# Optimization experiments

Measured on AMD Instinct MI355X. Metric: run time of the kernel, lower is better.

Reference implementation:

```python
import jax, jax.numpy as jnp
import numpy as np

H = 16  # n_heads

def setup_inputs() -> dict:
    key = jax.random.key(0)
    k1, k2, k3, k4 = jax.random.split(key, 4)
    B, S, D = 2, 2048, 1024
    query = jax.random.normal(k1, (B, S, D), dtype=jnp.float32)
    pos_emb = jax.random.normal(k2, (S, D), dtype=jnp.float32)
    w_qkv = jax.random.normal(k3, (D, 3 * D), dtype=jnp.float32) * (D ** -0.5)
    w_out = jax.random.normal(k4, (D, D), dtype=jnp.float32) * (D ** -0.5)
    return {"query": query, "pos_emb": pos_emb, "w_qkv": w_qkv, "w_out": w_out}

def reference(query, pos_emb, w_qkv, w_out):
    B, S, D = query.shape
    d_k = D // H
    # ape=True: pos_fn applied to input before QKV projection (additive APE)
    x = query + pos_emb[None, :, :]
    # fused QKV projection; torch view(B,S,H,3*d_k) + chunk(3,-1) == reshape(B,S,H,3,d_k)
    qkv = jnp.einsum('bsd,de->bse', x, w_qkv).reshape(B, S, H, 3, d_k)
    qkv = jnp.transpose(qkv, (0, 2, 1, 3, 4))  # [B,H,S,3,d_k]
    q, k, v = qkv[..., 0, :], qkv[..., 1, :], qkv[..., 2, :]
    scale = d_k ** -0.5
    scores = jnp.einsum('bhqd,bhkd->bhqk', q, k) * scale  # [B,H,S,S]
    attn = jax.nn.softmax(scores, axis=-1)  # dropout is identity in eval
    o = jnp.einsum('bhqk,bhkd->bhqd', attn, v)
    o = jnp.transpose(o, (0, 2, 1, 3)).reshape(B, S, D)
    return jnp.einsum('bsd,de->bse', o, w_out)
```

## Files before the change

kernel.cpp:

```cpp
#include <hip/hip_runtime.h>

#define SS 2048
#define DD 1024
#define N3 3072

typedef unsigned short u16;
typedef unsigned int u32;
typedef __attribute__((ext_vector_type(8))) short bf16x8;
typedef __attribute__((ext_vector_type(4))) short bf16x4;
typedef __attribute__((ext_vector_type(4))) float f32x4;

__device__ __forceinline__ u16 f2bf(float f) {
    u32 u = __float_as_uint(f);
    u32 r = u + 0x7fffu + ((u >> 16) & 1u);
    return (u16)(r >> 16);
}

__device__ __forceinline__ float fast_exp2(float x) {
    return __builtin_amdgcn_exp2f(x);
}

__device__ __forceinline__ void async_cp16(u16* lds, const u16* g) {
    __builtin_amdgcn_global_load_lds((const __attribute__((address_space(1))) u32*)g,
                                     (__attribute__((address_space(3))) u32*)lds, 16, 0, 0);
}

__device__ __forceinline__ f32x4 mfma16(bf16x4 a, bf16x4 b, f32x4 c) {
    return __builtin_amdgcn_mfma_f32_16x16x16bf16_1k(a, b, c, 0, 0, 0);
}

__global__ __launch_bounds__(256)
void prep_all(const float* __restrict__ q, const float* __restrict__ pos,
              const float* __restrict__ wqkv, const float* __restrict__ wout,
              u16* __restrict__ x, u16* __restrict__ wqkvT, u16* __restrict__ woutT)
{
    __shared__ float t[32][33];
    const int bx = blockIdx.x;

    if (bx < 4096) {
        const size_t i = ((size_t)bx * 256 + threadIdx.x) * 4;
        float4 a = *(const float4*)(q + i);
        float4 p = *(const float4*)(pos + (i & (size_t)(SS * DD - 1)));
        uint2 r;
        r.x = (u32)f2bf(a.x + p.x) | ((u32)f2bf(a.y + p.y) << 16);
        r.y = (u32)f2bf(a.z + p.z) | ((u32)f2bf(a.w + p.w) << 16);
        *(uint2*)(x + i) = r;
        return;
    }

    const int isq = bx < 7168;
    const int tt  = isq ? (bx - 4096) : (bx - 7168);
    const int nx  = isq ? 96 : 32;
    const int N   = isq ? N3 : DD;
    const float* W = isq ? wqkv : wout;
    u16* WT = isq ? wqkvT : woutT;

    const int x0 = (tt % nx) * 32, y0 = (tt / nx) * 32;
    const int tx = threadIdx.x & 31, ty = threadIdx.x >> 5;
#pragma unroll
    for (int i = 0; i < 4; ++i)
        t[ty + i * 8][tx] = W[(size_t)(y0 + ty + i * 8) * N + x0 + tx];
    __syncthreads();
#pragma unroll
    for (int i = 0; i < 4; ++i) {
        const int n = x0 + ty + i * 8;
        float v = t[tx][ty + i * 8];
        if (isq && (n % 192) < 64) v *= 0.18033688f;
        WT[(size_t)n * DD + y0 + tx] = f2bf(v);
    }
}

__global__ __launch_bounds__(256)
void transpose_v(const u16* __restrict__ qkv, u16* __restrict__ vt)
{
    __shared__ u16 t[64][72];
    const int bx = blockIdx.x;
    const int bh = bx >> 5, st = bx & 31;
    const int b = bh >> 4, h = bh & 15;
    const int r = threadIdx.x >> 2, c16 = (threadIdx.x & 3) * 16;

    const u16* src = qkv + (size_t)(b * SS + st * 64 + r) * N3 + h * 192 + 128 + c16;
    *(uint4*)&t[r][c16]     = *(const uint4*)src;
    *(uint4*)&t[r][c16 + 8] = *(const uint4*)(src + 8);
    __syncthreads();

    union { uint4 q[2]; u16 hh[16]; } u;
#pragma unroll
    for (int j = 0; j < 16; ++j) u.hh[j] = t[c16 + j][r];
    uint4* dst = (uint4*)(vt + ((size_t)bh * 64 + r) * SS + st * 64 + c16);
    dst[0] = u.q[0]; dst[1] = u.q[1];
}

__global__ __launch_bounds__(512, 2)
void gemm256(const u16* __restrict__ A, const u16* __restrict__ BT,
             u16* __restrict__ C, int M, int N, int K)
{
    extern __shared__ __align__(16) u16 smem[];

    const int tid = threadIdx.x;
    const int lane = tid & 63;
    const int wv = tid >> 6;
    const int quad = lane >> 4, l16 = lane & 15;
    const int wm = wv >> 2, wn = wv & 3;
    const int m0 = blockIdx.y * 256, n0 = blockIdx.x * 256;
    const int sw = l16 & 7;

    const int srow = tid >> 3, pc = tid & 7, lc = pc ^ (srow & 7);
    const u16* agp = A  + (size_t)(m0 + srow) * K + lc * 8;
    const u16* bgp = BT + (size_t)(n0 + srow) * K + lc * 8;
    u16* const asw = smem +         srow * 64 + pc * 8;
    u16* const bsw = smem + 32768 + srow * 64 + pc * 8;

    auto stage = [&](int buf, int k0) {
#pragma unroll
        for (int s = 0; s < 4; ++s)
            async_cp16(asw + buf * 16384 + s * 4096, agp + (size_t)(s * 64) * K + k0);
#pragma unroll
        for (int s = 0; s < 4; ++s)
            async_cp16(bsw + buf * 16384 + s * 4096, bgp + (size_t)(s * 64) * K + k0);
    };

    f32x4 acc[8][4];
#pragma unroll
    for (int i = 0; i < 8; ++i)
#pragma unroll
        for (int j = 0; j < 4; ++j) acc[i][j] = {0.f, 0.f, 0.f, 0.f};

    stage(0, 0);

    const int NT = K / 64;
    for (int t = 0; t < NT; ++t) {
        const int p = t & 1;
        asm volatile("s_waitcnt vmcnt(0) lgkmcnt(0)\n\ts_barrier" ::: "memory");
        if (t + 1 < NT) stage(p ^ 1, (t + 1) * 64);

        const u16* Ab = smem +         p * 16384;
        const u16* Bb = smem + 32768 + p * 16384;

#pragma unroll
        for (int ks = 0; ks < 2; ++ks) {
            bf16x8 bfr[4];
#pragma unroll
            for (int nt = 0; nt < 4; ++nt)
                bfr[nt] = *(const bf16x8*)&Bb[(wn * 64 + nt * 16 + l16) * 64 + (((ks * 4 + quad) ^ sw) << 3)];
#pragma unroll
            for (int mt = 0; mt < 8; ++mt) {
                bf16x8 af = *(const bf16x8*)&Ab[(wm * 128 + mt * 16 + l16) * 64 + (((ks * 4 + quad) ^ sw) << 3)];
#pragma unroll
                for (int nt = 0; nt < 4; ++nt)
                    acc[mt][nt] = __builtin_amdgcn_mfma_f32_16x16x32_bf16(af, bfr[nt], acc[mt][nt], 0, 0, 0);
            }
        }
    }

#pragma unroll
    for (int mt = 0; mt < 8; ++mt)
#pragma unroll
        for (int r = 0; r < 4; ++r) {
            const size_t row = m0 + wm * 128 + mt * 16 + quad * 4 + r;
            u16* cp = C + row * N + n0 + wn * 64 + l16;
#pragma unroll
            for (int nt = 0; nt < 4; ++nt) cp[nt * 16] = f2bf(acc[mt][nt][r]);
        }
}

template <int OUT_BF16, int NT>
__global__ __launch_bounds__(256)
void gemm_mfma(const u16* __restrict__ A, const u16* __restrict__ BT,
               void* __restrict__ Cv, int M, int N, int K)
{
    constexpr int FR = NT / 32;
    __shared__ u16 As[128 * 64];
    __shared__ u16 Bs[NT * 64];

    const int tid = threadIdx.x;
    const int lane = tid & 63, wv = tid >> 6;
    const int quad = lane >> 4, l16 = lane & 15;
    const int m0 = blockIdx.y * 128, n0 = blockIdx.x * NT;

    const int arow = wv * 32 + (lane >> 3);
    const int pc   = lane & 7;
    const int lcA  = pc ^ (arow & 7);
    const u16* agp = A + (size_t)(m0 + arow) * K + lcA * 8;
    u16* alp = As + arow * 64 + pc * 8;

    const int brow = (NT == 128) ? (wv * 32 + (lane >> 3)) : (wv * 8 + (lane >> 3));
    const int lcB  = pc ^ (brow & 7);
    const u16* bgp = BT + (size_t)(n0 + brow) * K + lcB * 8;
    u16* blp = Bs + brow * 64 + pc * 8;

    const int moff = (wv >> 1) * 64, noff = (wv & 1) * (NT / 2);

    f32x4 acc[4][FR];
#pragma unroll
    for (int i = 0; i < 4; ++i)
#pragma unroll
        for (int j = 0; j < FR; ++j) acc[i][j] = {0.f, 0.f, 0.f, 0.f};

    const int swf = l16 & 7;

    for (int k0 = 0; k0 < K; k0 += 64) {
#pragma unroll
        for (int s = 0; s < 4; ++s)
            async_cp16(alp + s * 8 * 64, agp + (size_t)(s * 8) * K + k0);
        if constexpr (NT == 128) {
#pragma unroll
            for (int s = 0; s < 4; ++s)
                async_cp16(blp + s * 8 * 64, bgp + (size_t)(s * 8) * K + k0);
        } else {
#pragma unroll
            for (int s = 0; s < 2; ++s)
                async_cp16(blp + s * 32 * 64, bgp + (size_t)(s * 32) * K + k0);
        }
        __syncthreads();

#pragma unroll
        for (int ks = 0; ks < 2; ++ks) {
            bf16x8 af[4], bfr[FR];
#pragma unroll
            for (int t = 0; t < 4; ++t)
                af[t] = *(const bf16x8*)&As[(moff + t * 16 + l16) * 64 + (((ks * 4 + quad) ^ swf) << 3)];
#pragma unroll
            for (int t = 0; t < FR; ++t)
                bfr[t] = *(const bf16x8*)&Bs[(noff + t * 16 + l16) * 64 + (((ks * 4 + quad) ^ swf) << 3)];
#pragma unroll
            for (int mt = 0; mt < 4; ++mt)
#pragma unroll
                for (int nt = 0; nt < FR; ++nt)
                    acc[mt][nt] = __builtin_amdgcn_mfma_f32_16x16x32_bf16(af[mt], bfr[nt], acc[mt][nt], 0, 0, 0);
        }
        __syncthreads();
    }

#pragma unroll
    for (int mt = 0; mt < 4; ++mt)
#pragma unroll
        for (int r = 0; r < 4; ++r) {
            const size_t row = m0 + moff + mt * 16 + quad * 4 + r;
            if (OUT_BF16) {
                u16* cp = (u16*)Cv + row * N + n0 + noff + l16;
#pragma unroll
                for (int nt = 0; nt < FR; ++nt) cp[nt * 16] = f2bf(acc[mt][nt][r]);
            } else {
                float* cp = (float*)Cv + row * N + n0 + noff + l16;
#pragma unroll
                for (int nt = 0; nt < FR; ++nt) cp[nt * 16] = acc[mt][nt][r];
            }
        }
}

__global__ __launch_bounds__(512, 4)
void attn_mfma(const u16* __restrict__ qkv, const u16* __restrict__ vt, u16* __restrict__ o)
{
    __shared__ __align__(16) u16 smem[32768];

    const int tid = threadIdx.x;
    const int lane = tid & 63, wv = tid >> 6;
    const int grp = wv >> 2, w4 = wv & 3;
    const int quad = lane >> 4, l16 = lane & 15;
    const int bx = blockIdx.x;
    const int bh = bx & 31, qt = bx >> 5;
    const int h = bh & 15, b = bh >> 4;

    const size_t hb = (size_t)b * SS * N3 + h * 192;
    const int q0 = qt * 128 + w4 * 32;
    const int sw = l16 & 7;

    bf16x8 qf[2][2];
#pragma unroll
    for (int mt = 0; mt < 2; ++mt)
#pragma unroll
        for (int ks = 0; ks < 2; ++ks)
            qf[mt][ks] = *(const bf16x8*)(qkv + hb + (size_t)(q0 + mt * 16 + l16) * N3 + ks * 32 + quad * 8);

    f32x4 po[2][4];
#pragma unroll
    for (int mt = 0; mt < 2; ++mt)
#pragma unroll
        for (int nt = 0; nt < 4; ++nt) po[mt][nt] = {0.f, 0.f, 0.f, 0.f};
    float lrun[2] = {0.f, 0.f};

    const int lrow = lane >> 3, pc8 = lane & 7, lc = pc8 ^ lrow;
    const int srow = w4 * 16;
    const int kt0 = grp * 16;

    const u16* kgp = qkv + hb + 64 + (size_t)(kt0 * 64 + srow + lrow) * N3 + lc * 8;
    const u16* vgp = vt + ((size_t)bh * 64 + srow + lrow) * SS + kt0 * 64 + lc * 8;

    u16* const ksA = smem + (grp * 2) * 4096 + (srow + lrow) * 64 + pc8 * 8;
    u16* const ksB = ksA + 4096;
    u16* const vsA = smem + 16384 + (grp * 2) * 4096 + (srow + lrow) * 64 + pc8 * 8;
    u16* const vsB = vsA + 4096;

    async_cp16(ksA,       kgp);
    async_cp16(ksA + 512, kgp + (size_t)8 * N3);
    async_cp16(vsA,       vgp);
    async_cp16(vsA + 512, vgp + (size_t)8 * SS);

    for (int it = 0; it < 16; ++it) {
        const int p = it & 1;
        asm volatile("s_waitcnt vmcnt(0) lgkmcnt(0)\n\ts_barrier" ::: "memory");
        if (it < 15) {
            const size_t ko = (size_t)(it + 1) * 64;
            u16* kb = p ? ksA : ksB;
            u16* vb = p ? vsA : vsB;
            async_cp16(kb,       kgp + ko * N3);
            async_cp16(kb + 512, kgp + ko * N3 + (size_t)8 * N3);
            async_cp16(vb,       vgp + ko);
            async_cp16(vb + 512, vgp + ko + (size_t)8 * SS);
        }
        const u16* kbuf = smem + (grp * 2 + p) * 4096;
        const u16* vbuf = smem + 16384 + (grp * 2 + p) * 4096;

        f32x4 sf[2][4];
#pragma unroll
        for (int mt = 0; mt < 2; ++mt)
#pragma unroll
            for (int kn = 0; kn < 4; ++kn) sf[mt][kn] = {0.f, 0.f, 0.f, 0.f};
        __builtin_amdgcn_s_setprio(1);
#pragma unroll
        for (int ks = 0; ks < 2; ++ks)
#pragma unroll
            for (int kn = 0; kn < 4; ++kn) {
                bf16x8 kf = *(const bf16x8*)&kbuf[(kn * 16 + l16) * 64 + (((ks * 4 + quad) ^ sw) << 3)];
#pragma unroll
                for (int mt = 0; mt < 2; ++mt)
                    sf[mt][kn] = __builtin_amdgcn_mfma_f32_16x16x32_bf16(kf, qf[mt][ks], sf[mt][kn], 0, 0, 0);
            }
        __builtin_amdgcn_s_setprio(0);

        u32 SW[2][4][2];
#pragma unroll
        for (int mt = 0; mt < 2; ++mt) {
            float ls = 0.f;
#pragma unroll
            for (int kn = 0; kn < 4; ++kn) {
                const float p0 = fast_exp2(sf[mt][kn][0]);
                const float p1 = fast_exp2(sf[mt][kn][1]);
                const float p2 = fast_exp2(sf[mt][kn][2]);
                const float p3 = fast_exp2(sf[mt][kn][3]);
                ls += (p0 + p1) + (p2 + p3);
                SW[mt][kn][0] = __builtin_amdgcn_perm(__float_as_uint(p1), __float_as_uint(p0), 0x07060302u);
                SW[mt][kn][1] = __builtin_amdgcn_perm(__float_as_uint(p3), __float_as_uint(p2), 0x07060302u);
            }
            lrun[mt] += ls;
        }

        __builtin_amdgcn_s_setprio(1);
#pragma unroll
        for (int kn = 0; kn < 4; ++kn) {
            bf16x4 vf[4];
#pragma unroll
            for (int nt = 0; nt < 4; ++nt)
                vf[nt] = *(const bf16x4*)&vbuf[(nt * 16 + l16) * 64 + (((2 * kn + (quad >> 1)) ^ sw) << 3) + ((quad & 1) << 2)];
#pragma unroll
            for (int mt = 0; mt < 2; ++mt) {
                union { bf16x4 v; u32 w[2]; } pu;
                pu.w[0] = SW[mt][kn][0];
                pu.w[1] = SW[mt][kn][1];
#pragma unroll
                for (int nt = 0; nt < 4; ++nt)
                    po[mt][nt] = mfma16(vf[nt], pu.v, po[mt][nt]);
            }
        }
        __builtin_amdgcn_s_setprio(0);
    }

    __syncthreads();

#pragma unroll
    for (int mt = 0; mt < 2; ++mt) {
        lrun[mt] += __shfl_xor(lrun[mt], 16, 64);
        lrun[mt] += __shfl_xor(lrun[mt], 32, 64);
    }

    float* xch = (float*)smem;
    if (grp == 1) {
        float* d = xch + (w4 * 64 + lane) * 36;
#pragma unroll
        for (int mt = 0; mt < 2; ++mt)
#pragma unroll
            for (int nt = 0; nt < 4; ++nt)
                *(f32x4*)(d + mt * 16 + nt * 4) = po[mt][nt];
        d[32] = lrun[0]; d[33] = lrun[1];
    }
    __syncthreads();
    if (grp == 0) {
        const float* s = xch + (w4 * 64 + lane) * 36;
#pragma unroll
        for (int mt = 0; mt < 2; ++mt)
#pragma unroll
            for (int nt = 0; nt < 4; ++nt)
                po[mt][nt] = po[mt][nt] + *(const f32x4*)(s + mt * 16 + nt * 4);
        lrun[0] += s[32]; lrun[1] += s[33];

#pragma unroll
        for (int mt = 0; mt < 2; ++mt) {
            const float linv = 1.f / lrun[mt];
            const size_t row = (size_t)b * SS + q0 + mt * 16 + l16;
#pragma unroll
            for (int nt = 0; nt < 4; ++nt) {
                const u32 h0 = (u32)f2bf(po[mt][nt][0] * linv) | ((u32)f2bf(po[mt][nt][1] * linv) << 16);
                const u32 h1 = (u32)f2bf(po[mt][nt][2] * linv) | ((u32)f2bf(po[mt][nt][3] * linv) << 16);
                uint2 wp; wp.x = h0; wp.y = h1;
                *(uint2*)(o + row * DD + h * 64 + nt * 16 + quad * 4) = wp;
            }
        }
    }
}

extern "C" void kernel_launch(void* const* d_in, const int* in_sizes, int n_in,
                              void* d_out, int out_size, void* d_ws, size_t ws_size,
                              hipStream_t stream)
{
    const float* query  = (const float*)d_in[0];
    const float* posemb = (const float*)d_in[1];
    const float* w_qkv  = (const float*)d_in[2];
    const float* w_out  = (const float*)d_in[3];
    float* out = (float*)d_out;

    u16* xb    = (u16*)d_ws;
    u16* wqkvT = xb    + (size_t)4096 * 1024;
    u16* woutT = wqkvT + (size_t)3072 * 1024;
    u16* qkv   = woutT + (size_t)1024 * 1024;
    u16* ob    = qkv   + (size_t)4096 * 3072;
    u16* vtb   = ob    + (size_t)4096 * 1024;

    static bool lds_init = false;
    if (!lds_init) {
        hipFuncSetAttribute((const void*)gemm256,
                            hipFuncAttributeMaxDynamicSharedMemorySize, 131072);
        lds_init = true;
    }

    prep_all<<<8192, 256, 0, stream>>>(query, posemb, w_qkv, w_out, xb, wqkvT, woutT);

    gemm256<<<dim3(N3 / 256, 4096 / 256), 512, 131072, stream>>>(xb, wqkvT, qkv, 4096, N3, DD);

    transpose_v<<<1024, 256, 0, stream>>>(qkv, vtb);

    attn_mfma<<<dim3(512, 1, 1), 512, 0, stream>>>(qkv, vtb, ob);

    gemm_mfma<0, 64><<<dim3(DD / 64, 4096 / 128), 256, 0, stream>>>(ob, woutT, (void*)out, 4096, DD, DD);
}
```

Measured before the change: 185.2 us.

## Fuse V transpose into QKV GEMM epilogue, regroup weight columns, swizzle blocks

Result: no change. 184.7 us (-0.3%).

```diff
diff --git a/kernel.cpp b/kernel.cpp
--- a/kernel.cpp
+++ b/kernel.cpp
@@ -64,45 +64,36 @@
 #pragma unroll
     for (int i = 0; i < 4; ++i) {
         const int n = x0 + ty + i * 8;
+        int dst = n;
+        if (isq) {
+            const int hh = n / 192, r = n % 192;
+            dst = (r < 64) ? hh * 64 + r
+                : (r < 128) ? 1024 + hh * 64 + (r - 64)
+                            : 2048 + hh * 64 + (r - 128);
+        }
         float v = t[tx][ty + i * 8];
-        if (isq && (n % 192) < 64) v *= 0.18033688f;
-        WT[(size_t)n * DD + y0 + tx] = f2bf(v);
-    }
-}
-
-__global__ __launch_bounds__(256)
-void transpose_v(const u16* __restrict__ qkv, u16* __restrict__ vt)
-{
-    __shared__ u16 t[64][72];
-    const int bx = blockIdx.x;
-    const int bh = bx >> 5, st = bx & 31;
-    const int b = bh >> 4, h = bh & 15;
-    const int r = threadIdx.x >> 2, c16 = (threadIdx.x & 3) * 16;
-
-    const u16* src = qkv + (size_t)(b * SS + st * 64 + r) * N3 + h * 192 + 128 + c16;
-    *(uint4*)&t[r][c16]     = *(const uint4*)src;
-    *(uint4*)&t[r][c16 + 8] = *(const uint4*)(src + 8);
-    __syncthreads();
-
-    union { uint4 q[2]; u16 hh[16]; } u;
-#pragma unroll
-    for (int j = 0; j < 16; ++j) u.hh[j] = t[c16 + j][r];
-    uint4* dst = (uint4*)(vt + ((size_t)bh * 64 + r) * SS + st * 64 + c16);
-    dst[0] = u.q[0]; dst[1] = u.q[1];
+        if (isq && dst < 1024) v *= 0.18033688f;
+        WT[(size_t)dst * DD + y0 + tx] = f2bf(v);
+    }
 }
 
 __global__ __launch_bounds__(512, 2)
 void gemm256(const u16* __restrict__ A, const u16* __restrict__ BT,
-             u16* __restrict__ C, int M, int N, int K)
+             u16* __restrict__ C, u16* __restrict__ vt, int M, int N, int K, int nbx)
 {
     extern __shared__ __align__(16) u16 smem[];
+
+    const int bid = blockIdx.x;
+    const int chunk = (int)gridDim.x >> 3;
+    const int swz = (bid & 7) * chunk + (bid >> 3);
+    const int bxs = swz % nbx, bys = swz / nbx;
 
     const int tid = threadIdx.x;
     const int lane = tid & 63;
     const int wv = tid >> 6;
     const int quad = lane >> 4, l16 = lane & 15;
     const int wm = wv >> 2, wn = wv & 3;
-    const int m0 = blockIdx.y * 256, n0 = blockIdx.x * 256;
+    const int m0 = bys * 256, n0 = bxs * 256;
     const int sw = l16 & 7;
 
     const int srow = tid >> 3, pc = tid & 7, lc = pc ^ (srow & 7);
@@ -153,30 +144,61 @@
         }
     }
 
-#pragma unroll
-    for (int mt = 0; mt < 8; ++mt)
-#pragma unroll
-        for (int r = 0; r < 4; ++r) {
-            const size_t row = m0 + wm * 128 + mt * 16 + quad * 4 + r;
-            u16* cp = C + row * N + n0 + wn * 64 + l16;
-#pragma unroll
-            for (int nt = 0; nt < 4; ++nt) cp[nt * 16] = f2bf(acc[mt][nt][r]);
-        }
+    if (vt && n0 >= 2048) {
+        __syncthreads();
+        u16* tb = smem;
+#pragma unroll
+        for (int mt = 0; mt < 8; ++mt)
+#pragma unroll
+            for (int nt = 0; nt < 4; ++nt) {
+                const int vl = wn * 64 + nt * 16 + l16;
+                const int ml = wm * 128 + mt * 16 + quad * 4;
+                uint2 w;
+                w.x = (u32)f2bf(acc[mt][nt][0]) | ((u32)f2bf(acc[mt][nt][1]) << 16);
+                w.y = (u32)f2bf(acc[mt][nt][2]) | ((u32)f2bf(acc[mt][nt][3]) << 16);
+                *(uint2*)(tb + (size_t)vl * 264 + ml) = w;
+            }
+        __syncthreads();
+        const int vl = tid >> 1, half = tid & 1;
+        const int b16 = (m0 >> 11) * 16;
+        const int hh = ((n0 - 2048) >> 6) + (vl >> 6);
+        const int dk = vl & 63;
+        u16* dst = vt + ((size_t)(b16 + hh) * 64 + dk) * SS + (m0 & 2047) + half * 128;
+        const u16* src = tb + (size_t)vl * 264 + half * 128;
+#pragma unroll
+        for (int j = 0; j < 16; ++j)
+            *(uint4*)(dst + j * 8) = *(const uint4*)(src + j * 8);
+    } else {
+#pragma unroll
+        for (int mt = 0; mt < 8; ++mt)
+#pragma unroll
+            for (int r = 0; r < 4; ++r) {
+                const size_t row = m0 + wm * 128 + mt * 16 + quad * 4 + r;
+                u16* cp = C + row * N + n0 + wn * 64 + l16;
+#pragma unroll
+                for (int nt = 0; nt < 4; ++nt) cp[nt * 16] = f2bf(acc[mt][nt][r]);
+            }
+    }
 }
 
 template <int OUT_BF16, int NT>
 __global__ __launch_bounds__(256)
 void gemm_mfma(const u16* __restrict__ A, const u16* __restrict__ BT,
-               void* __restrict__ Cv, int M, int N, int K)
+               void* __restrict__ Cv, int M, int N, int K, int nbx)
 {
     constexpr int FR = NT / 32;
     __shared__ u16 As[128 * 64];
     __shared__ u16 Bs[NT * 64];
 
+    const int bid = blockIdx.x;
+    const int chunk = (int)gridDim.x >> 3;
+    const int swz = (bid & 7) * chunk + (bid >> 3);
+    const int bxs = swz % nbx, bys = swz / nbx;
+
     const int tid = threadIdx.x;
     const int lane = tid & 63, wv = tid >> 6;
     const int quad = lane >> 4, l16 = lane & 15;
-    const int m0 = blockIdx.y * 128, n0 = blockIdx.x * NT;
+    const int m0 = bys * 128, n0 = bxs * NT;
 
     const int arow = wv * 32 + (lane >> 3);
     const int pc   = lane & 7;
@@ -262,7 +284,7 @@
     const int bh = bx & 31, qt = bx >> 5;
     const int h = bh & 15, b = bh >> 4;
 
-    const size_t hb = (size_t)b * SS * N3 + h * 192;
+    const size_t base = (size_t)b * SS * N3;
     const int q0 = qt * 128 + w4 * 32;
     const int sw = l16 & 7;
 
@@ -271,7 +293,7 @@
     for (int mt = 0; mt < 2; ++mt)
 #pragma unroll
         for (int ks = 0; ks < 2; ++ks)
-            qf[mt][ks] = *(const bf16x8*)(qkv + hb + (size_t)(q0 + mt * 16 + l16) * N3 + ks * 32 + quad * 8);
+            qf[mt][ks] = *(const bf16x8*)(qkv + base + h * 64 + (size_t)(q0 + mt * 16 + l16) * N3 + ks * 32 + quad * 8);
 
     f32x4 po[2][4];
 #pragma unroll
@@ -284,7 +306,7 @@
     const int srow = w4 * 16;
     const int kt0 = grp * 16;
 
-    const u16* kgp = qkv + hb + 64 + (size_t)(kt0 * 64 + srow + lrow) * N3 + lc * 8;
+    const u16* kgp = qkv + base + 1024 + h * 64 + (size_t)(kt0 * 64 + srow + lrow) * N3 + lc * 8;
     const u16* vgp = vt + ((size_t)bh * 64 + srow + lrow) * SS + kt0 * 64 + lc * 8;
 
     u16* const ksA = smem + (grp * 2) * 4096 + (srow + lrow) * 64 + pc8 * 8;
@@ -429,17 +451,15 @@
     static bool lds_init = false;
     if (!lds_init) {
         hipFuncSetAttribute((const void*)gemm256,
-                            hipFuncAttributeMaxDynamicSharedMemorySize, 131072);
+                            hipFuncAttributeMaxDynamicSharedMemorySize, 135168);
         lds_init = true;
     }
 
     prep_all<<<8192, 256, 0, stream>>>(query, posemb, w_qkv, w_out, xb, wqkvT, woutT);
 
-    gemm256<<<dim3(N3 / 256, 4096 / 256), 512, 131072, stream>>>(xb, wqkvT, qkv, 4096, N3, DD);
-
-    transpose_v<<<1024, 256, 0, stream>>>(qkv, vtb);
+    gemm256<<<192, 512, 135168, stream>>>(xb, wqkvT, qkv, vtb, 4096, N3, DD, N3 / 256);
 
     attn_mfma<<<dim3(512, 1, 1), 512, 0, stream>>>(qkv, vtb, ob);
 
-    gemm_mfma<0, 64><<<dim3(DD / 64, 4096 / 128), 256, 0, stream>>>(ob, woutT, (void*)out, 4096, DD, DD);
-}
+    gemm_mfma<0, 64><<<512, 256, 0, stream>>>(ob, woutT, (void*)out, 4096, DD, DD, DD / 64);
+}
```

## Retile QKV GEMM to 128x192 tiles, reorder QKV columns, swizzle block IDs

Applied to the files above, without the earlier changes.

Result: no change. 186.5 us (+0.7%).

```diff
diff --git a/kernel.cpp b/kernel.cpp
--- a/kernel.cpp
+++ b/kernel.cpp
@@ -64,9 +64,16 @@
 #pragma unroll
     for (int i = 0; i < 4; ++i) {
         const int n = x0 + ty + i * 8;
+        int dst = n;
+        if (isq) {
+            const int hh = n / 192, r = n % 192;
+            dst = (r < 64) ? hh * 64 + r
+                : (r < 128) ? 1024 + hh * 64 + (r - 64)
+                            : 2048 + hh * 64 + (r - 128);
+        }
         float v = t[tx][ty + i * 8];
-        if (isq && (n % 192) < 64) v *= 0.18033688f;
-        WT[(size_t)n * DD + y0 + tx] = f2bf(v);
+        if (isq && dst < 1024) v *= 0.18033688f;
+        WT[(size_t)dst * DD + y0 + tx] = f2bf(v);
     }
 }
 
@@ -79,7 +86,7 @@
     const int b = bh >> 4, h = bh & 15;
     const int r = threadIdx.x >> 2, c16 = (threadIdx.x & 3) * 16;
 
-    const u16* src = qkv + (size_t)(b * SS + st * 64 + r) * N3 + h * 192 + 128 + c16;
+    const u16* src = qkv + (size_t)(b * SS + st * 64 + r) * N3 + 2048 + h * 64 + c16;
     *(uint4*)&t[r][c16]     = *(const uint4*)src;
     *(uint4*)&t[r][c16 + 8] = *(const uint4*)(src + 8);
     __syncthreads();
@@ -92,39 +99,44 @@
 }
 
 __global__ __launch_bounds__(512, 2)
-void gemm256(const u16* __restrict__ A, const u16* __restrict__ BT,
-             u16* __restrict__ C, int M, int N, int K)
+void gemm192(const u16* __restrict__ A, const u16* __restrict__ BT,
+             u16* __restrict__ C, int M, int N, int K, int nbx)
 {
     extern __shared__ __align__(16) u16 smem[];
+
+    const int bid = blockIdx.x;
+    const int chunk = (int)gridDim.x >> 3;
+    const int swz = (bid & 7) * chunk + (bid >> 3);
+    const int bxs = swz % nbx, bys = swz / nbx;
 
     const int tid = threadIdx.x;
     const int lane = tid & 63;
     const int wv = tid >> 6;
     const int quad = lane >> 4, l16 = lane & 15;
     const int wm = wv >> 2, wn = wv & 3;
-    const int m0 = blockIdx.y * 256, n0 = blockIdx.x * 256;
+    const int m0 = bys * 128, n0 = bxs * 192;
     const int sw = l16 & 7;
 
     const int srow = tid >> 3, pc = tid & 7, lc = pc ^ (srow & 7);
     const u16* agp = A  + (size_t)(m0 + srow) * K + lc * 8;
     const u16* bgp = BT + (size_t)(n0 + srow) * K + lc * 8;
     u16* const asw = smem +         srow * 64 + pc * 8;
-    u16* const bsw = smem + 32768 + srow * 64 + pc * 8;
+    u16* const bsw = smem + 16384 + srow * 64 + pc * 8;
 
     auto stage = [&](int buf, int k0) {
 #pragma unroll
-        for (int s = 0; s < 4; ++s)
-            async_cp16(asw + buf * 16384 + s * 4096, agp + (size_t)(s * 64) * K + k0);
-#pragma unroll
-        for (int s = 0; s < 4; ++s)
-            async_cp16(bsw + buf * 16384 + s * 4096, bgp + (size_t)(s * 64) * K + k0);
+        for (int s = 0; s < 2; ++s)
+            async_cp16(asw + buf * 8192 + s * 4096, agp + (size_t)(s * 64) * K + k0);
+#pragma unroll
+        for (int s = 0; s < 3; ++s)
+            async_cp16(bsw + buf * 12288 + s * 4096, bgp + (size_t)(s * 64) * K + k0);
     };
 
-    f32x4 acc[8][4];
-#pragma unroll
-    for (int i = 0; i < 8; ++i)
-#pragma unroll
-        for (int j = 0; j < 4; ++j) acc[i][j] = {0.f, 0.f, 0.f, 0.f};
+    f32x4 acc[4][3];
+#pragma unroll
+    for (int i = 0; i < 4; ++i)
+#pragma unroll
+        for (int j = 0; j < 3; ++j) acc[i][j] = {0.f, 0.f, 0.f, 0.f};
 
     stage(0, 0);
 
@@ -134,49 +146,57 @@
         asm volatile("s_waitcnt vmcnt(0) lgkmcnt(0)\n\ts_barrier" ::: "memory");
         if (t + 1 < NT) stage(p ^ 1, (t + 1) * 64);
 
-        const u16* Ab = smem +         p * 16384;
-        const u16* Bb = smem + 32768 + p * 16384;
+        const u16* Ab = smem +         p * 8192;
+        const u16* Bb = smem + 16384 + p * 12288;
 
 #pragma unroll
         for (int ks = 0; ks < 2; ++ks) {
-            bf16x8 bfr[4];
-#pragma unroll
-            for (int nt = 0; nt < 4; ++nt)
-                bfr[nt] = *(const bf16x8*)&Bb[(wn * 64 + nt * 16 + l16) * 64 + (((ks * 4 + quad) ^ sw) << 3)];
-#pragma unroll
-            for (int mt = 0; mt < 8; ++mt) {
-                bf16x8 af = *(const bf16x8*)&Ab[(wm * 128 + mt * 16 + l16) * 64 + (((ks * 4 + quad) ^ sw) << 3)];
-#pragma unroll
-                for (int nt = 0; nt < 4; ++nt)
-                    acc[mt][nt] = __builtin_amdgcn_mfma_f32_16x16x32_bf16(af, bfr[nt], acc[mt][nt], 0, 0, 0);
-            }
-        }
-    }
-
-#pragma unroll
-    for (int mt = 0; mt < 8; ++mt)
+            bf16x8 bfr[3], af[4];
+#pragma unroll
+            for (int nt = 0; nt < 3; ++nt)
+                bfr[nt] = *(const bf16x8*)&Bb[(wn * 48 + nt * 16 + l16) * 64 + (((ks * 4 + quad) ^ sw) << 3)];
+#pragma unroll
+            for (int mt = 0; mt < 4; ++mt)
+                af[mt] = *(const bf16x8*)&Ab[(wm * 64 + mt * 16 + l16) * 64 + (((ks * 4 + quad) ^ sw) << 3)];
+            __builtin_amdgcn_s_setprio(1);
+#pragma unroll
+            for (int mt = 0; mt < 4; ++mt)
+#pragma unroll
+                for (int nt = 0; nt < 3; ++nt)
+                    acc[mt][nt] = __builtin_amdgcn_mfma_f32_16x16x32_bf16(af[mt], bfr[nt], acc[mt][nt], 0, 0, 0);
+            __builtin_amdgcn_s_setprio(0);
+        }
+    }
+
+#pragma unroll
+    for (int mt = 0; mt < 4; ++mt)
 #pragma unroll
         for (int r = 0; r < 4; ++r) {
-            const size_t row = m0 + wm * 128 + mt * 16 + quad * 4 + r;
-            u16* cp = C + row * N + n0 + wn * 64 + l16;
-#pragma unroll
-            for (int nt = 0; nt < 4; ++nt) cp[nt * 16] = f2bf(acc[mt][nt][r]);
+            const size_t row = m0 + wm * 64 + mt * 16 + quad * 4 + r;
+            u16* cp = C + row * N + n0 + wn * 48 + l16;
+#pragma unroll
+            for (int nt = 0; nt < 3; ++nt) cp[nt * 16] = f2bf(acc[mt][nt][r]);
         }
 }
 
 template <int OUT_BF16, int NT>
 __global__ __launch_bounds__(256)
 void gemm_mfma(const u16* __restrict__ A, const u16* __restrict__ BT,
-               void* __restrict__ Cv, int M, int N, int K)
+               void* __restrict__ Cv, int M, int N, int K, int nbx)
 {
     constexpr int FR = NT / 32;
     __shared__ u16 As[128 * 64];
     __shared__ u16 Bs[NT * 64];
 
+    const int bid = blockIdx.x;
+    const int chunk = (int)gridDim.x >> 3;
+    const int swz = (bid & 7) * chunk + (bid >> 3);
+    const int bxs = swz % nbx, bys = swz / nbx;
+
     const int tid = threadIdx.x;
     const int lane = tid & 63, wv = tid >> 6;
     const int quad = lane >> 4, l16 = lane & 15;
-    const int m0 = blockIdx.y * 128, n0 = blockIdx.x * NT;
+    const int m0 = bys * 128, n0 = bxs * NT;
 
     const int arow = wv * 32 + (lane >> 3);
     const int pc   = lane & 7;
@@ -262,7 +282,7 @@
     const int bh = bx & 31, qt = bx >> 5;
     const int h = bh & 15, b = bh >> 4;
 
-    const size_t hb = (size_t)b * SS * N3 + h * 192;
+    const size_t base = (size_t)b * SS * N3;
     const int q0 = qt * 128 + w4 * 32;
     const int sw = l16 & 7;
 
@@ -271,7 +291,7 @@
     for (int mt = 0; mt < 2; ++mt)
 #pragma unroll
         for (int ks = 0; ks < 2; ++ks)
-            qf[mt][ks] = *(const bf16x8*)(qkv + hb + (size_t)(q0 + mt * 16 + l16) * N3 + ks * 32 + quad * 8);
+            qf[mt][ks] = *(const bf16x8*)(qkv + base + h * 64 + (size_t)(q0 + mt * 16 + l16) * N3 + ks * 32 + quad * 8);
 
     f32x4 po[2][4];
 #pragma unroll
@@ -284,7 +304,7 @@
     const int srow = w4 * 16;
     const int kt0 = grp * 16;
 
-    const u16* kgp = qkv + hb + 64 + (size_t)(kt0 * 64 + srow + lrow) * N3 + lc * 8;
+    const u16* kgp = qkv + base + 1024 + h * 64 + (size_t)(kt0 * 64 + srow + lrow) * N3 + lc * 8;
     const u16* vgp = vt + ((size_t)bh * 64 + srow + lrow) * SS + kt0 * 64 + lc * 8;
 
     u16* const ksA = smem + (grp * 2) * 4096 + (srow + lrow) * 64 + pc8 * 8;
@@ -428,18 +448,18 @@
 
     static bool lds_init = false;
     if (!lds_init) {
-        hipFuncSetAttribute((const void*)gemm256,
-                            hipFuncAttributeMaxDynamicSharedMemorySize, 131072);
+        hipFuncSetAttribute((const void*)gemm192,
+                            hipFuncAttributeMaxDynamicSharedMemorySize, 81920);
         lds_init = true;
     }
 
     prep_all<<<8192, 256, 0, stream>>>(query, posemb, w_qkv, w_out, xb, wqkvT, woutT);
 
-    gemm256<<<dim3(N3 / 256, 4096 / 256), 512, 131072, stream>>>(xb, wqkvT, qkv, 4096, N3, DD);
+    gemm192<<<512, 512, 81920, stream>>>(xb, wqkvT, qkv, 4096, N3, DD, N3 / 192);
 
     transpose_v<<<1024, 256, 0, stream>>>(qkv, vtb);
 
     attn_mfma<<<dim3(512, 1, 1), 512, 0, stream>>>(qkv, vtb, ob);
 
-    gemm_mfma<0, 64><<<dim3(DD / 64, 4096 / 128), 256, 0, stream>>>(ob, woutT, (void*)out, 4096, DD, DD);
-}
+    gemm_mfma<0, 64><<<512, 256, 0, stream>>>(ob, woutT, (void*)out, 4096, DD, DD, DD / 64);
+}
```
